# Kernel tuning notes

Hardware: AMD Instinct MI355X
Metric: run time of the kernel (lower is better)

## Reference

```python
import jax, jax.numpy as jnp
import numpy as np
import math

B, T, C = 4, 2048, 1024
N_HEAD = 16
HEAD = C // N_HEAD  # 64
ROPE_BASE = 10000.0


def rotate_half(x):
    x1, x2 = x[..., : x.shape[-1] // 2], x[..., x.shape[-1] // 2:]
    return jnp.concatenate((-x2, x1), axis=-1)


def rope_cos_sin(seq_len, dim, dtype=jnp.float32):
    inv_freq = 1.0 / (ROPE_BASE ** (jnp.arange(0, dim, 2, dtype=jnp.float32) / dim))
    t = jnp.arange(seq_len, dtype=jnp.float32)
    freqs = jnp.einsum('i,j->ij', t, inv_freq)          # [T, dim/2]
    emb = jnp.concatenate((freqs, freqs), axis=-1)       # [T, dim]
    return jnp.cos(emb).astype(dtype), jnp.sin(emb).astype(dtype)


def setup_inputs() -> dict:
    key = jax.random.key(0)
    ks = jax.random.split(key, 5)
    s_in = 1.0 / math.sqrt(C)
    return {
        'x': jax.random.normal(ks[0], (B, T, C), dtype=jnp.float32),
        'W_qkv': jax.random.normal(ks[1], (C, 3 * C), dtype=jnp.float32) * s_in,
        'b_qkv': jnp.zeros((3 * C,), dtype=jnp.float32),
        'W_proj': jax.random.normal(ks[2], (C, C), dtype=jnp.float32) * s_in,
        'b_proj': jnp.zeros((C,), dtype=jnp.float32),
    }


def reference(x, W_qkv, b_qkv, W_proj, b_proj):
    b, t, c = x.shape
    qkv = x @ W_qkv + b_qkv                               # [B,T,3C]
    q, k, v = jnp.split(qkv, 3, axis=-1)
    # [B,T,C] -> [B,H,T,hd]
    def to_heads(u):
        return u.reshape(b, t, N_HEAD, HEAD).transpose(0, 2, 1, 3)
    q, k, v = to_heads(q), to_heads(k), to_heads(v)
    # RoPE
    cos, sin = rope_cos_sin(t, HEAD, x.dtype)             # [T,hd]
    cos = cos[None, None]; sin = sin[None, None]
    q = q * cos + rotate_half(q) * sin
    k = k * cos + rotate_half(k) * sin
    # naive causal attention (materializes [B,H,T,T] like the original)
    att = jnp.einsum('bhqd,bhkd->bhqk', q, k) * (1.0 / math.sqrt(HEAD))
    causal = jnp.tril(jnp.ones((t, t), dtype=bool))
    att = jnp.where(causal[None, None], att, -jnp.inf)
    att = jax.nn.softmax(att, axis=-1)
    y = jnp.einsum('bhqk,bhkd->bhqd', att, v)             # [B,H,T,hd]
    y = y.transpose(0, 2, 1, 3).reshape(b, t, c)
    return y @ W_proj + b_proj
```

## Files before the change

### kernel.cpp

```cpp
#include <hip/hip_runtime.h>
#include <stdint.h>

#define B_  4
#define T_  2048
#define C_  1024
#define NH_ 16
#define HD_ 64
#define BH_ (B_*NH_)
#define M_  (B_*T_)

using f32x4  = __attribute__((ext_vector_type(4))) float;
using f32x16 = __attribute__((ext_vector_type(16))) float;
using bf16x8 = __attribute__((ext_vector_type(8))) short;

__device__ __forceinline__ unsigned short f2bf(float x) {
  union { float f; uint32_t u; } v; v.f = x;
  uint32_t u = v.u;
  return (unsigned short)((u + 0x7FFFu + ((u >> 16) & 1u)) >> 16);
}

__device__ __forceinline__ uint32_t cvtpk(float a, float b) {
  uint32_t r;
  asm("v_cvt_pk_bf16_f32 %0, %1, %2" : "=v"(r) : "v"(a), "v"(b));
  return r;
}

__device__ __forceinline__ void gload16(const void* g, void* l) {
  __builtin_amdgcn_global_load_lds(
      (const __attribute__((address_space(1))) void*)g,
      (__attribute__((address_space(3))) void*)l, 16, 0, 0);
}

#define BAR() do { asm volatile("" ::: "memory"); __builtin_amdgcn_s_barrier(); \
                   asm volatile("" ::: "memory"); } while (0)
#define VMC(N) asm volatile("s_waitcnt vmcnt(" #N ")" ::: "memory")


__global__ void k_cvt_bf16(const float* __restrict__ src,
                           unsigned short* __restrict__ dst, int n) {
  int i = (blockIdx.x * 256 + threadIdx.x) * 4;
  if (i + 3 < n) {
    float4 v = *(const float4*)(src + i);
    ushort4 o;
    o.x = f2bf(v.x); o.y = f2bf(v.y); o.z = f2bf(v.z); o.w = f2bf(v.w);
    *(ushort4*)(dst + i) = o;
  }
}

__global__ void k_transpose_w(const float* __restrict__ W,
                              unsigned short* __restrict__ WT, int K, int N) {
  __shared__ float tile[32][33];
  int bx = blockIdx.x, by = blockIdx.y;
  int tx = threadIdx.x, ty = threadIdx.y;
  #pragma unroll
  for (int i = 0; i < 32; i += 8)
    tile[ty + i][tx] = W[(size_t)(by*32 + ty + i) * N + bx*32 + tx];
  __syncthreads();
  #pragma unroll
  for (int i = 0; i < 32; i += 8)
    WT[(size_t)(bx*32 + ty + i) * K + by*32 + tx] = f2bf(tile[tx][ty + i]);
}

__global__ void k_rope_tab(float* __restrict__ cosT, float* __restrict__ sinT) {
  int t = blockIdx.x * 8 + threadIdx.y;
  int i = threadIdx.x;
  float inv = expf(-(float)i * (9.210340371976184f / 32.0f));
  float f = (float)t * inv;
  cosT[t*32 + i] = cosf(f);
  sinT[t*32 + i] = sinf(f);
}

template<int N, int K, int EPI>
__global__ __launch_bounds__(256, 3)
void k_gemm(const unsigned short* __restrict__ Ag,
            const unsigned short* __restrict__ BT,
            const float* __restrict__ bias,
            const float* __restrict__ cosT,
            const float* __restrict__ sinT,
            unsigned short* __restrict__ Qh,
            unsigned short* __restrict__ Kh,
            unsigned short* __restrict__ VhT,
            float* __restrict__ outF) {
  __shared__ alignas(16) unsigned short As[2][128*32];
  __shared__ alignas(16) unsigned short Bs[2][128*32];
  const int tid  = threadIdx.x;
  const int lane = tid & 63;
  const int wv   = tid >> 6;
  const int wm   = wv >> 1, wn = wv & 1;
  const int l15  = lane & 15, l4 = lane >> 4;
  const int NT  = N / 128;
  const int id  = ((int)blockIdx.x & 7) * ((int)gridDim.x >> 3) + ((int)blockIdx.x >> 3);
  const int m0  = (id / NT) * 128;
  const int n0  = (id % NT) * 128;

  f32x4 acc[4][4] = {};

  const int ga = l4 ^ (l15 & 3);
  const unsigned short* aR0 = &As[0][(wm*64 + l15)*32 + ga*8];
  const unsigned short* aR1 = &As[1][(wm*64 + l15)*32 + ga*8];
  const unsigned short* bR0 = &Bs[0][(wn*64 + l15)*32 + ga*8];
  const unsigned short* bR1 = &Bs[1][(wn*64 + l15)*32 + ga*8];

  const int srow = tid >> 2;
  const int sg   = (tid & 3) ^ (srow & 3);
  const int voff = srow*K + sg*8;
  const int ldsD = wv*512;
  const unsigned short* Abase = Ag + (size_t)m0*K;
  const unsigned short* Bbase = BT + (size_t)n0*K;

#define STG(BUF, KT) do { \
  const int _u = (KT)*32; \
  gload16(Abase + (0*64*K + _u) + voff, (void*)(&As[BUF][0*2048 + ldsD])); \
  gload16(Abase + (1*64*K + _u) + voff, (void*)(&As[BUF][1*2048 + ldsD])); \
  gload16(Bbase + (0*64*K + _u) + voff, (void*)(&Bs[BUF][0*2048 + ldsD])); \
  gload16(Bbase + (1*64*K + _u) + voff, (void*)(&Bs[BUF][1*2048 + ldsD])); \
} while (0)

#define CMP(AR, BR) do { \
  bf16x8 afr[4], bfr[4]; \
  _Pragma("unroll") for (int mi = 0; mi < 4; ++mi) \
    afr[mi] = *(const bf16x8*)((AR) + mi*512); \
  _Pragma("unroll") for (int ni = 0; ni < 4; ++ni) \
    bfr[ni] = *(const bf16x8*)((BR) + ni*512); \
  __builtin_amdgcn_s_setprio(1); \
  _Pragma("unroll") for (int mi = 0; mi < 4; ++mi) \
  _Pragma("unroll") for (int ni = 0; ni < 4; ++ni) \
    acc[mi][ni] = __builtin_amdgcn_mfma_f32_16x16x32_bf16( \
        afr[mi], bfr[ni], acc[mi][ni], 0, 0, 0); \
  __builtin_amdgcn_s_setprio(0); \
} while (0)

  STG(0, 0);
  #pragma unroll 1
  for (int i = 0; i < K/64; ++i) {
    STG(1, 2*i + 1);
    VMC(4);
    BAR();
    CMP(aR0, bR0);
    BAR();
    if (i + 1 < K/64) {
      STG(0, 2*i + 2);
      VMC(4);
    } else {
      VMC(0);
    }
    BAR();
    CMP(aR1, bR1);
    BAR();
  }
#undef STG
#undef CMP

  if (EPI == 0) {
    const int ncol = n0 + wn*64;
    const int part = ncol >> 10;
    const int hid  = (ncol & 1023) >> 6;
    unsigned short* dstQK = (part == 0) ? Qh : Kh;
    #pragma unroll
    for (int mi = 0; mi < 4; ++mi) {
      #pragma unroll
      for (int j = 0; j < 4; ++j) {
        int row = m0 + wm*64 + mi*16 + l4*4 + j;
        int bb = row >> 11, tt = row & 2047;
        if (part < 2) {
          size_t base = ((size_t)((bb*NH_ + hid) * T_ + tt)) * HD_;
          #pragma unroll
          for (int ni = 0; ni < 2; ++ni) {
            int d = ni*16 + l15;
            float a1 = acc[mi][ni][j]     + bias[ncol + d];
            float a2 = acc[mi][ni + 2][j] + bias[ncol + d + 32];
            float cv = cosT[tt*32 + d], sv = sinT[tt*32 + d];
            float o1 = a1*cv - a2*sv;
            float o2 = a2*cv + a1*sv;
            if (part == 0) { o1 *= 0.18033688011112042f; o2 *= 0.18033688011112042f; }
            dstQK[base + d]      = f2bf(o1);
            dstQK[base + d + 32] = f2bf(o2);
          }
        } else {
          #pragma unroll
          for (int ni = 0; ni < 4; ++ni) {
            int d = ni*16 + l15;
            float av = acc[mi][ni][j] + bias[ncol + d];
            VhT[((size_t)((bb*NH_ + hid) * HD_ + d)) * T_ + tt] = f2bf(av);
          }
        }
      }
    }
  } else {
    #pragma unroll
    for (int mi = 0; mi < 4; ++mi)
      #pragma unroll
      for (int ni = 0; ni < 4; ++ni)
        #pragma unroll
        for (int j = 0; j < 4; ++j) {
          int row = m0 + wm*64 + mi*16 + l4*4 + j;
          int col = n0 + wn*64 + ni*16 + l15;
          outF[(size_t)row * N + col] = acc[mi][ni][j] + bias[col];
        }
  }
}

__global__ __launch_bounds__(256, 3)
void k_attn(const unsigned short* __restrict__ Qh,
            const unsigned short* __restrict__ Kh,
            const unsigned short* __restrict__ VhT,
            unsigned short* __restrict__ Y) {
  __shared__ alignas(16) unsigned short Ks[2][64*64];
  __shared__ alignas(16) unsigned short Vs[2][64*64];
  const int tid  = threadIdx.x;
  const int lane = tid & 63;
  const int wv   = tid >> 6;
  const int l31  = lane & 31;
  const int h    = lane >> 5;
  const int bh   = blockIdx.x & 63;
  const int qb   = 15 - (blockIdx.x >> 6);
  const int r32  = qb*128 + wv*32;
  const int nt   = 2*qb + 2;
  const int qg   = r32 + l31;

  bf16x8 qf[4];
  #pragma unroll
  for (int i = 0; i < 4; ++i)
    qf[i] = *(const bf16x8*)(Qh + ((size_t)(bh*T_ + qg))*HD_ + i*16 + h*8);

  float m_r = -1e30f, l_r = 0.f;
  f32x16 o[2] = {};

  auto stage = [&](int buf, int jt) {
    #pragma unroll
    for (int it = 0; it < 2; ++it) {
      int idx = it*256 + wv*64 + lane;
      int row = idx >> 3, slot = idx & 7;
      int g   = slot ^ (row & 7);
      gload16(Kh  + ((size_t)(bh*T_ + jt*64 + row))*HD_ + g*8,
              (void*)(Ks[buf] + (it*256 + wv*64)*8));
      gload16(VhT + ((size_t)(bh*HD_ + row))*T_ + jt*64 + g*8,
              (void*)(Vs[buf] + (it*256 + wv*64)*8));
    }
  };

  stage(0, 0);
  int cur = 0;

  for (int jt = 0; jt < nt; ++jt) {
    if (jt + 1 < nt) {
      stage(cur ^ 1, jt + 1);
      VMC(4);
    } else {
      VMC(0);
    }
    BAR();

    if (jt*64 <= r32 + 31) {
      f32x16 s[2] = {f32x16{0}, f32x16{0}};
      __builtin_amdgcn_s_setprio(1);
      #pragma unroll
      for (int kb = 0; kb < 2; ++kb)
        #pragma unroll
        for (int i = 0; i < 4; ++i) {
          int r = kb*32 + l31;
          int g = (2*i + h) ^ (r & 7);
          bf16x8 kf = *(const bf16x8*)(Ks[cur] + r*64 + g*8);
          s[kb] = __builtin_amdgcn_mfma_f32_32x32x16_bf16(kf, qf[i], s[kb], 0, 0, 0);
        }
      __builtin_amdgcn_s_setprio(0);

      float p[2][16];
      const bool diag = (jt + 1)*64 > r32;
      #pragma unroll
      for (int kb = 0; kb < 2; ++kb)
        #pragma unroll
        for (int r = 0; r < 16; ++r) {
          float v = s[kb][r];
          if (diag) {
            int key = jt*64 + kb*32 + (r & 3) + 8*(r >> 2) + 4*h;
            v = (key > qg) ? -1e30f : v;
          }
          p[kb][r] = v;
        }

      float mx[16];
      #pragma unroll
      for (int r = 0; r < 16; ++r) mx[r] = fmaxf(p[0][r], p[1][r]);
      #pragma unroll
      for (int st = 8; st > 0; st >>= 1)
        #pragma unroll
        for (int r = 0; r < 8; ++r)
          if (r < st) mx[r] = fmaxf(mx[r], mx[r + st]);
      float tm = fmaxf(mx[0], __shfl_xor(mx[0], 32));

      if (!__all(tm <= m_r + 8.0f)) {
        float mn = fmaxf(m_r, tm);
        float scale = exp2f(m_r - mn);
        m_r = mn;
        l_r *= scale;
        #pragma unroll
        for (int dblk = 0; dblk < 2; ++dblk)
          #pragma unroll
          for (int r = 0; r < 16; ++r)
            o[dblk][r] *= scale;
      }

      #pragma unroll
      for (int kb = 0; kb < 2; ++kb)
        #pragma unroll
        for (int r = 0; r < 16; ++r)
          p[kb][r] = exp2f(p[kb][r] - m_r);

      float sm[16];
      #pragma unroll
      for (int r = 0; r < 16; ++r) sm[r] = p[0][r] + p[1][r];
      #pragma unroll
      for (int st = 8; st > 0; st >>= 1)
        #pragma unroll
        for (int r = 0; r < 8; ++r)
          if (r < st) sm[r] += sm[r + st];
      l_r += sm[0] + __shfl_xor(sm[0], 32);

      #pragma unroll
      for (int kb = 0; kb < 2; ++kb) {
        uint32_t a01 = cvtpk(p[kb][0],  p[kb][1]);
        uint32_t a23 = cvtpk(p[kb][2],  p[kb][3]);
        uint32_t a45 = cvtpk(p[kb][4],  p[kb][5]);
        uint32_t a67 = cvtpk(p[kb][6],  p[kb][7]);
        uint32_t b01 = cvtpk(p[kb][8],  p[kb][9]);
        uint32_t b23 = cvtpk(p[kb][10], p[kb][11]);
        uint32_t b45 = cvtpk(p[kb][12], p[kb][13]);
        uint32_t b67 = cvtpk(p[kb][14], p[kb][15]);
        uint32_t s1 = h ? a01 : a45, s2 = h ? a23 : a67;
        uint32_t s3 = h ? b01 : b45, s4 = h ? b23 : b67;
        uint32_t x1 = __shfl_xor(s1, 32), x2 = __shfl_xor(s2, 32);
        uint32_t x3 = __shfl_xor(s3, 32), x4 = __shfl_xor(s4, 32);
        union { bf16x8 v; uint32_t d[4]; } f0, f1;
        f0.d[0] = h ? x1 : a01;  f0.d[1] = h ? x2 : a23;
        f0.d[2] = h ? a45 : x1;  f0.d[3] = h ? a67 : x2;
        f1.d[0] = h ? x3 : b01;  f1.d[1] = h ? x4 : b23;
        f1.d[2] = h ? b45 : x3;  f1.d[3] = h ? b67 : x4;

        __builtin_amdgcn_s_setprio(1);
        #pragma unroll
        for (int koff = 0; koff < 2; ++koff) {
          bf16x8 pf = koff ? f1.v : f0.v;
          #pragma unroll
          for (int dblk = 0; dblk < 2; ++dblk) {
            int rv = dblk*32 + l31;
            int gv = (kb*4 + koff*2 + h) ^ (rv & 7);
            bf16x8 vf = *(const bf16x8*)(Vs[cur] + rv*64 + gv*8);
            o[dblk] = __builtin_amdgcn_mfma_f32_32x32x16_bf16(vf, pf, o[dblk], 0, 0, 0);
          }
        }
        __builtin_amdgcn_s_setprio(0);
      }
    }

    BAR();
    cur ^= 1;
  }

  int b = bh >> 4, hd = bh & 15;
  float rinv = 1.0f / l_r;
  unsigned short* yrow = Y + ((size_t)(b*T_ + r32 + l31))*C_ + hd*64;
  #pragma unroll
  for (int dblk = 0; dblk < 2; ++dblk)
    #pragma unroll
    for (int g2 = 0; g2 < 4; ++g2) {
      ushort4 o4;
      o4.x = f2bf(o[dblk][g2*4 + 0] * rinv);
      o4.y = f2bf(o[dblk][g2*4 + 1] * rinv);
      o4.z = f2bf(o[dblk][g2*4 + 2] * rinv);
      o4.w = f2bf(o[dblk][g2*4 + 3] * rinv);
      *(ushort4*)(yrow + dblk*32 + g2*8 + 4*h) = o4;
    }
}


extern "C" void kernel_launch(void* const* d_in, const int* in_sizes, int n_in,
                              void* d_out, int out_size, void* d_ws, size_t ws_size,
                              hipStream_t stream) {
  const float* x      = (const float*)d_in[0];
  const float* W_qkv  = (const float*)d_in[1];
  const float* b_qkv  = (const float*)d_in[2];
  const float* W_proj = (const float*)d_in[3];
  const float* b_proj = (const float*)d_in[4];
  float* out = (float*)d_out;

  char* ws = (char*)d_ws;
  size_t off = 0;
  auto alloc = [&](size_t bytes) {
    void* p = ws + off; off += (bytes + 255) & ~(size_t)255; return p;
  };
  unsigned short* xb     = (unsigned short*)alloc((size_t)M_ * C_ * 2);
  unsigned short* WqkvT  = (unsigned short*)alloc((size_t)3 * C_ * C_ * 2);
  unsigned short* WprojT = (unsigned short*)alloc((size_t)C_ * C_ * 2);
  unsigned short* Qh     = (unsigned short*)alloc((size_t)M_ * C_ * 2);
  unsigned short* Kh     = (unsigned short*)alloc((size_t)M_ * C_ * 2);
  unsigned short* VhT    = (unsigned short*)alloc((size_t)M_ * C_ * 2);
  float* cosT = (float*)alloc((size_t)T_ * 32 * 4);
  float* sinT = (float*)alloc((size_t)T_ * 32 * 4);
  unsigned short* Y = xb;

  k_cvt_bf16<<<(M_*C_/4 + 255)/256, 256, 0, stream>>>(x, xb, M_*C_);
  dim3 tb(32, 8);
  k_transpose_w<<<dim3(3*C_/32, C_/32), tb, 0, stream>>>(W_qkv, WqkvT, C_, 3*C_);
  k_transpose_w<<<dim3(C_/32,   C_/32), tb, 0, stream>>>(W_proj, WprojT, C_, C_);
  k_rope_tab<<<T_/8, tb, 0, stream>>>(cosT, sinT);

  k_gemm<3*C_, C_, 0><<<dim3(1536), 256, 0, stream>>>(
      xb, WqkvT, b_qkv, cosT, sinT, Qh, Kh, VhT, nullptr);

  k_attn<<<dim3(T_/128 * BH_), 256, 0, stream>>>(Qh, Kh, VhT, Y);

  k_gemm<C_, C_, 1><<<dim3(512), 256, 0, stream>>>(
      Y, WprojT, b_proj, nullptr, nullptr, nullptr, nullptr, nullptr, out);
}
```

Measured before the change: 210.8 us.

## Deepen GEMM LDS pipeline to four stages with stronger swizzle

The GEMM mainloop moves from a 2-buffer to a 4-buffer LDS ring, keeping three k-tiles of global loads in flight ahead of compute so memory latency is better hidden. The XOR swizzle also gains an extra term to cut LDS bank conflicts on fragment reads. LDS use doubles to 64KB per block and the launch bound drops to 2 blocks per SM, which trades occupancy for prefetch depth.

```diff
diff --git a/kernel.cpp b/kernel.cpp
--- a/kernel.cpp
+++ b/kernel.cpp
@@ -71,7 +71,7 @@
 }
 
 template<int N, int K, int EPI>
-__global__ __launch_bounds__(256, 3)
+__global__ __launch_bounds__(256, 2)
 void k_gemm(const unsigned short* __restrict__ Ag,
             const unsigned short* __restrict__ BT,
             const float* __restrict__ bias,
@@ -81,8 +81,8 @@
             unsigned short* __restrict__ Kh,
             unsigned short* __restrict__ VhT,
             float* __restrict__ outF) {
-  __shared__ alignas(16) unsigned short As[2][128*32];
-  __shared__ alignas(16) unsigned short Bs[2][128*32];
+  __shared__ alignas(16) unsigned short As[4][128*32];
+  __shared__ alignas(16) unsigned short Bs[4][128*32];
   const int tid  = threadIdx.x;
   const int lane = tid & 63;
   const int wv   = tid >> 6;
@@ -95,14 +95,19 @@
 
   f32x4 acc[4][4] = {};
 
-  const int ga = l4 ^ (l15 & 3);
-  const unsigned short* aR0 = &As[0][(wm*64 + l15)*32 + ga*8];
-  const unsigned short* aR1 = &As[1][(wm*64 + l15)*32 + ga*8];
-  const unsigned short* bR0 = &Bs[0][(wn*64 + l15)*32 + ga*8];
-  const unsigned short* bR1 = &Bs[1][(wn*64 + l15)*32 + ga*8];
+  const int fr = (l15 & 3) ^ ((l15 >> 2) & 3);
+  const int sA = l4 ^ fr;
+  const unsigned short* aP0 = &As[0][(wm*64 + l15)*32 + sA*8];
+  const unsigned short* aP1 = &As[1][(wm*64 + l15)*32 + sA*8];
+  const unsigned short* aP2 = &As[2][(wm*64 + l15)*32 + sA*8];
+  const unsigned short* aP3 = &As[3][(wm*64 + l15)*32 + sA*8];
+  const unsigned short* bP0 = &Bs[0][(wn*64 + l15)*32 + sA*8];
+  const unsigned short* bP1 = &Bs[1][(wn*64 + l15)*32 + sA*8];
+  const unsigned short* bP2 = &Bs[2][(wn*64 + l15)*32 + sA*8];
+  const unsigned short* bP3 = &Bs[3][(wn*64 + l15)*32 + sA*8];
 
   const int srow = tid >> 2;
-  const int sg   = (tid & 3) ^ (srow & 3);
+  const int sg   = (tid & 3) ^ (srow & 3) ^ ((srow >> 2) & 3);
   const int voff = srow*K + sg*8;
   const int ldsD = wv*512;
   const unsigned short* Abase = Ag + (size_t)m0*K;
@@ -130,23 +135,18 @@
   __builtin_amdgcn_s_setprio(0); \
 } while (0)
 
-  STG(0, 0);
+  STG(0, 0); STG(1, 1); STG(2, 2);
   #pragma unroll 1
-  for (int i = 0; i < K/64; ++i) {
-    STG(1, 2*i + 1);
-    VMC(4);
-    BAR();
-    CMP(aR0, bR0);
-    BAR();
-    if (i + 1 < K/64) {
-      STG(0, 2*i + 2);
-      VMC(4);
-    } else {
-      VMC(0);
-    }
-    BAR();
-    CMP(aR1, bR1);
-    BAR();
+  for (int i = 0; i < K/128; ++i) {
+    const int t = 4*i;
+    STG(3, t + 3);  VMC(12);
+    BAR();  CMP(aP0, bP0);  BAR();
+    if (i + 1 < K/128) { STG(0, t + 4); VMC(12); } else VMC(8);
+    BAR();  CMP(aP1, bP1);  BAR();
+    if (i + 1 < K/128) { STG(1, t + 5); VMC(12); } else VMC(4);
+    BAR();  CMP(aP2, bP2);  BAR();
+    if (i + 1 < K/128) { STG(2, t + 6); VMC(12); } else VMC(0);
+    BAR();  CMP(aP3, bP3);  BAR();
   }
 #undef STG
 #undef CMP
```

New measurement: 221.1 us. +4.9%, slower.
